# Kernel tuning notes

Measured on AMD Instinct MI355X. Metric: run time of the kernel, lower is better.

## Reference

```python
import jax, jax.numpy as jnp
import numpy as np
from jax import lax

B, T, C, H, W = 2, 5, 2, 128, 256
E, M, L = 64, 16, 4  # embedding_dim, n_fno_modes, n_fno_layers
EPS = 1e-5


def conv1x1(x, w, b):
    # x: [N, I, H, W], w: [O, I], b: [O]
    return jnp.einsum('nihw,oi->nohw', x, w) + b[None, :, None, None]


def conv3x3(x, w, b):
    # x: [N, I, H, W], w: [O, I, 3, 3]
    y = lax.conv_general_dilated(x, w, window_strides=(1, 1), padding='SAME',
                                 dimension_numbers=('NCHW', 'OIHW', 'NCHW'))
    return y + b[None, :, None, None]


def instance_norm(x):
    # InstanceNorm2d(affine=False): normalize over H,W per (n, c), biased var
    mu = jnp.mean(x, axis=(2, 3), keepdims=True)
    var = jnp.var(x, axis=(2, 3), keepdims=True)
    return (x - mu) * lax.rsqrt(var + EPS)


def upsample2x_nearest(x):
    return jnp.repeat(jnp.repeat(x, 2, axis=2), 2, axis=3)


def resize_nearest(x, out_h, out_w):
    # torch F.interpolate mode='nearest': idx = floor(i * in / out)
    in_h, in_w = x.shape[2], x.shape[3]
    hi = (jnp.arange(out_h) * in_h) // out_h
    wi = (jnp.arange(out_w) * in_w) // out_w
    return x[:, :, hi, :][:, :, :, wi]


def fno_layer(x, wr, wi, cw, cb):
    # x: [N, E, H, W]; wr/wi: [2, E, E, M, M]; cw: [E, E]; cb: [E]
    h, w = x.shape[2], x.shape[3]
    coeff = jnp.fft.rfft2(x, axes=(2, 3), norm='ortho')  # [N, E, H, W//2+1]
    w0 = wr[0] + 1j * wi[0]
    w1 = wr[1] + 1j * wi[1]
    out = jnp.zeros_like(coeff)
    out = out.at[:, :, :M, :M].set(
        jnp.einsum('nixy,ioxy->noxy', coeff[:, :, :M, :M], w0))
    out = out.at[:, :, -M:, :M].set(
        jnp.einsum('nixy,ioxy->noxy', coeff[:, :, -M:, :M], w1))
    spec = jnp.fft.irfft2(out, s=(h, w), axes=(2, 3), norm='ortho')
    return jax.nn.gelu(conv1x1(x, cw, cb) + spec, approximate=False)


def setup_inputs() -> dict:
    key = jax.random.key(0)
    ks = jax.random.split(key, 10)
    s = 0.02
    return {
        'sensor_value': jax.random.normal(ks[0], (B, T, C, H, W), jnp.float32),
        'updim_w': 0.3 * jax.random.normal(ks[1], (E, C), jnp.float32),
        'updim_b': jnp.zeros((E,), jnp.float32),
        'smooth_w': 0.04 * jax.random.normal(ks[2], (E, E, 3, 3), jnp.float32),
        'smooth_b': jnp.zeros((E,), jnp.float32),
        'fno_wr': s * jax.random.normal(ks[3], (L, 2, E, E, M, M), jnp.float32),
        'fno_wi': s * jax.random.normal(ks[4], (L, 2, E, E, M, M), jnp.float32),
        'fno_cw': 0.1 * jax.random.normal(ks[5], (L, E, E), jnp.float32),
        'fno_cb': jnp.zeros((L, E), jnp.float32),
        'downdim_w': 0.1 * jax.random.normal(ks[6], (C, E), jnp.float32),
        'downdim_b': jnp.zeros((C,), jnp.float32),
    }


def reference(sensor_value, updim_w, updim_b, smooth_w, smooth_b,
              fno_wr, fno_wi, fno_cw, fno_cb, downdim_w, downdim_b):
    b, t, c, h, w = sensor_value.shape
    x = sensor_value.reshape(b * t, c, h, w)
    x = conv1x1(x, updim_w, updim_b)
    x = upsample2x_nearest(x)
    x = jax.nn.gelu(instance_norm(conv3x3(x, smooth_w, smooth_b)), approximate=False)
    x = resize_nearest(x, H, W)
    for l in range(L):
        x = fno_layer(x, fno_wr[l], fno_wi[l], fno_cw[l], fno_cb[l])
    x = conv1x1(x, downdim_w, downdim_b)
    return x.reshape(b, t, c, H, W)
```

## Files before the change

### kernel.cpp

```cpp
#include <hip/hip_runtime.h>
#include <math.h>

#define PI_D 3.14159265358979323846


typedef _Float16 h8 __attribute__((ext_vector_type(8)));
typedef float f16v __attribute__((ext_vector_type(16)));

__device__ __forceinline__ float gelu_f(float v){
  return 0.5f*v*(1.0f + erff(v*0.70710678118654752440f));
}

__device__ __forceinline__ int fsw_c(int w){ return (w ^ (w >> 3)) & 7; }

__global__ __launch_bounds__(256) void k_tables(float* __restrict__ twFwH, float* __restrict__ twBwH,
                                                _Float16* __restrict__ Tspec, _Float16* __restrict__ TdftW){
  int id = blockIdx.x*256 + threadIdx.x;
  if (id < 4096){
    int h = id >> 5, m = id & 31;
    int xm = (m < 16) ? m : (96 + m);
    double ang = -2.0*PI_D*(double)((xm*h) & 127)/128.0;
    twFwH[id*2]   = (float)cos(ang);
    twFwH[id*2+1] = (float)sin(ang);
  } else if (id < 8192){
    int j = id - 4096;
    int h = j >> 5, m = j & 31;
    int xm = (m < 16) ? m : (96 + m);
    double ang = 2.0*PI_D*(double)((xm*h) & 127)/128.0;
    twBwH[j*2]   = (float)cos(ang);
    twBwH[j*2+1] = (float)sin(ang);
  } else if (id < 16384){
    int j = id - 8192;
    int w = j >> 5, kk = j & 31;
    int y = kk >> 1;
    double ang = 2.0*PI_D*(double)((w*y) & 255)/256.0;
    double v = (kk & 1) ? -sin(ang) : cos(ang);
    Tspec[j] = (_Float16)v;
  } else if (id < 24576){
    int j = id - 16384;
    int y2 = j >> 8, w = j & 255;
    int y = y2 >> 1;
    double ang = -2.0*PI_D*(double)((w*y) & 255)/256.0;
    double v = (y2 & 1) ? sin(ang) : cos(ang);
    TdftW[j] = (_Float16)v;
  }
}

__global__ __launch_bounds__(256) void k_foldK(const float* __restrict__ smw, const float* __restrict__ upw,
                                               const float* __restrict__ upb, float* __restrict__ Keff){
  int id = blockIdx.x*256 + threadIdx.x;
  if (id >= 1024) return;
  int o = id >> 4, rs = (id >> 2) & 3, tap = id & 3;
  int r = rs >> 1, s = rs & 1, a = tap >> 1, b = tap & 1;
  int klo = (r==0) ? (a==0?0:1) : (a==0?0:2);
  int khi = (r==0) ? (a==0?0:2) : (a==0?1:2);
  int llo = (s==0) ? (b==0?0:1) : (b==0?0:2);
  int lhi = (s==0) ? (b==0?0:2) : (b==0?1:2);
  float a0=0.f, a1=0.f, ab=0.f;
  for (int i=0;i<64;++i){
    float t = 0.f;
    for (int kh=klo; kh<=khi; ++kh)
      for (int kw=llo; kw<=lhi; ++kw)
        t += smw[((size_t)o*64+i)*9 + kh*3+kw];
    a0 += t*upw[i*2];
    a1 += t*upw[i*2+1];
    ab += t*upb[i];
  }
  *(float4*)(Keff + o*64 + (rs*4+tap)*4) = make_float4(a0, a1, ab, 0.f);
}

__global__ __launch_bounds__(256) void k_transW(const float* __restrict__ wr, const float* __restrict__ wi,
                                                unsigned* __restrict__ Wt){
  __shared__ unsigned P[64*257];
  int lb = blockIdx.x;
  int i = lb & 63, blk = (lb>>6)&1, l = lb>>7;
  int tid = threadIdx.x;
  size_t sbase = (size_t)l*2097152 + (size_t)blk*1048576 + (size_t)i*16384 + tid;
  for (int o=0;o<64;++o){
    float a = wr[sbase + (size_t)o*256];
    float b = wi[sbase + (size_t)o*256];
    union { unsigned u; _Float16 h[2]; } pk;
    pk.h[0] = (_Float16)a; pk.h[1] = (_Float16)b;
    P[o*257 + tid] = pk.u;
  }
  __syncthreads();
  int o = tid & 63, g = tid >> 6;
  size_t dbase = (size_t)(l*2+blk)*1048576;
  for (int it=0; it<64; ++it){
    int my = g*64 + it;
    Wt[dbase + (size_t)my*4096 + i*64 + o] = P[o*257 + my];
  }
}

__global__ __launch_bounds__(512) void k_corr(const float* __restrict__ sv, float* __restrict__ Rpart){
  __shared__ float S[2][6][260];
  int bid = blockIdx.x;
  int band = bid & 31, n = bid >> 5;
  int u0 = band*4;
  int tid = threadIdx.x;
  for (int t = tid; t < 3120; t += 512){
    int ch = t / 1560; int rem = t - ch*1560; int rr = rem / 260; int ci = rem - rr*260;
    int row = u0 - 1 + rr, col = ci - 1;
    float v = 0.f;
    if (row >= 0 && row < 128 && col >= 0 && col < 256)
      v = sv[((size_t)(n*2+ch)*128 + row)*256 + col];
    S[ch][rr][ci] = v;
  }
  __syncthreads();

  int lane = tid & 63, wv = tid >> 6;
  int c  = (wv<4) ? (wv>>1) : ((wv<6) ? (wv-4) : 2);
  int c2 = (wv<4) ? (wv&1)  : ((wv<6) ? 2 : (wv-6));
  float acc[9];
  #pragma unroll
  for (int k=0;k<9;++k) acc[k]=0.f;

  for (int r=0;r<4;++r){
    int u = u0 + r, lu = r + 1;
    for (int cb=0;cb<4;++cb){
      int v = cb*64 + lane;
      float f = (c==2) ? 1.f : S[c][lu][1+v];
      #pragma unroll
      for (int dr=-1;dr<=1;++dr){
        int ur = u + dr;
        float rko = (ur>=0 && ur<128) ? 1.f : 0.f;
        #pragma unroll
        for (int dc=-1;dc<=1;++dc){
          float g;
          if (c2==2){
            int vc = v + dc;
            g = rko * ((vc>=0 && vc<256) ? 1.f : 0.f);
          } else {
            g = S[c2][lu+dr][1+v+dc];
          }
          acc[(dr+1)*3 + dc+1] += f*g;
        }
      }
    }
  }
  #pragma unroll
  for (int k=0;k<9;++k){
    float v = acc[k];
    for (int off=32; off; off>>=1) v += __shfl_xor(v, off);
    if (lane==0) Rpart[((size_t)(n*32+band)*8 + wv)*9 + k] = v;
  }
}

__global__ __launch_bounds__(256) void k_bnd(const float* __restrict__ sv, float* __restrict__ Bnd){
  __shared__ float E[4][3][260];
  int n = blockIdx.x, tid = threadIdx.x;
  for (int t = tid; t < 3120; t += 256){
    int e = t/780; int rem = t - e*780; int ch = rem/260; int i = rem - ch*260;
    int idx = i - 1;
    int len = (e<2) ? 256 : 128;
    float v = 0.f;
    if (idx >= 0 && idx < len){
      if (ch==2) v = 1.f;
      else {
        int row = (e==0) ? 0 : (e==1) ? 127 : idx;
        int col = (e==2) ? 0 : (e==3) ? 255 : idx;
        v = sv[((size_t)(n*2+ch)*128 + row)*256 + col];
      }
    }
    E[e][ch][i] = v;
  }
  __syncthreads();
  if (tid < 108){
    int e = tid/27; int rem = tid - e*27; int pair = rem/3; int lag = rem%3 - 1;
    int c = pair/3, c2 = pair%3;
    int len = (e<2) ? 256 : 128;
    float a = 0.f;
    for (int i=0;i<len;++i) a += E[e][c][1+i]*E[e][c2][1+i+lag];
    Bnd[n*144 + tid] = a;
  } else if (tid < 144){
    int t = tid - 108; int corner = t/9; int pair = t - corner*9;
    int c = pair/3, c2 = pair%3;
    int e = (corner<2) ? 0 : 1;
    int idx = (corner&1) ? 255 : 0;
    Bnd[n*144 + tid] = E[e][c][1+idx]*E[e][c2][1+idx];
  }
}

__global__ __launch_bounds__(256) void k_stats3(const float* __restrict__ Rpart, const float* __restrict__ Bnd,
                                                const float* __restrict__ Keff, float* __restrict__ stats){
  __shared__ float R[9][9];
  __shared__ float BL[4][9][3];
  __shared__ float CR[4][9];
  __shared__ float M[4][12][12];
  int n = blockIdx.x, tid = threadIdx.x;

  if (tid < 72){
    int wv = tid/9, k = tid - (tid/9)*9;
    double s = 0.0;
    for (int b=0;b<32;++b) s += (double)Rpart[((size_t)(n*32+b)*8 + wv)*9 + k];
    int c  = (wv<4) ? (wv>>1) : ((wv<6) ? (wv-4) : 2);
    int c2 = (wv<4) ? (wv&1)  : ((wv<6) ? 2 : (wv-6));
    R[c*3+c2][k] = (float)s;
  } else if (tid < 81){
    int k = tid - 72; int dr = k/3 - 1, dc = k%3 - 1;
    R[8][k] = (float)((128 - (dr<0?-dr:dr)) * (256 - (dc<0?-dc:dc)));
  }
  if (tid < 108){
    int e = tid/27, rem = tid - (tid/27)*27;
    BL[e][rem/3][rem%3] = Bnd[n*144 + tid];
  } else if (tid < 144){
    int t = tid - 108;
    CR[t/9][t - (t/9)*9] = Bnd[n*144 + tid];
  }
  __syncthreads();

  for (int t = tid; t < 576; t += 256){
    int rs = t/144; int rem = t - rs*144; int i = rem/12, j = rem - (rem/12)*12;
    int ab = i/3,  c  = i - ab*3,  a  = ab>>1, b  = ab&1;
    int ab2 = j/3, c2 = j - ab2*3, a2 = ab2>>1, b2 = ab2&1;
    int r = rs>>1, s = rs&1;
    int dr = a2 - a, dc = b2 - b;
    int pair = c*3 + c2;
    float g = R[pair][(dr+1)*3 + (dc+1)];
    if (r==1 && a==1 && a2==1) g -= BL[0][pair][dc+1];
    if (r==0 && a==0 && a2==0) g -= BL[1][pair][dc+1];
    if (s==1 && b==1 && b2==1) g -= BL[2][pair][dr+1];
    if (s==0 && b==0 && b2==0) g -= BL[3][pair][dr+1];
    bool rowc = (a==a2) && ((r==1 && a==1) || (r==0 && a==0));
    bool colc = (b==b2) && ((s==1 && b==1) || (s==0 && b==0));
    if (rowc && colc){
      int corner = ((r==1)?0:2) + ((s==1)?0:1);
      g += CR[corner][pair];
    }
    M[rs][i][j] = g;
  }
  __syncthreads();

  if (tid < 64){
    int o = tid;
    double S1 = 0.0, S2 = 0.0;
    for (int rs=0; rs<4; ++rs){
      float w[12];
      #pragma unroll
      for (int ab=0; ab<4; ++ab){
        float4 kv = *(const float4*)(Keff + o*64 + (rs*4+ab)*4);
        w[ab*3+0] = kv.x; w[ab*3+1] = kv.y; w[ab*3+2] = kv.z;
      }
      #pragma unroll
      for (int i=0;i<12;++i){
        double ti = 0.0;
        #pragma unroll
        for (int j=0;j<12;++j) ti += (double)M[rs][i][j]*(double)w[j];
        S2 += (double)w[i]*ti;
      }
      #pragma unroll
      for (int ab=0; ab<4; ++ab)
        #pragma unroll
        for (int c=0;c<3;++c)
          S1 += (double)w[ab*3+c]*(double)M[rs][ab*3+c][ab*3+2];
    }
    double mu  = S1 / 131072.0;
    double var = S2 / 131072.0 - mu*mu;
    stats[(n*64+o)*2]   = (float)mu;
    stats[(n*64+o)*2+1] = (float)(1.0/sqrt(var + 1e-5));
  }
}

__global__ __launch_bounds__(256) void k_convnorm(const float* __restrict__ sv,
                                                  const float* __restrict__ Keff,
                                                  const float* __restrict__ stats,
                                                  _Float16* __restrict__ act){
  __shared__ float SV[4*260];
  int bid = blockIdx.x;
  int p = bid & 127, n = bid >> 7;
  int tid = threadIdx.x;
  for (int t = tid; t < 1032; t += 256){
    int dr = t / 516;
    int rem = t - dr*516;
    int ch = rem / 258;
    int ci = rem - ch*258;
    int row = p - 1 + dr;
    int col = ci - 1;
    float v = 0.f;
    if (row >= 0 && col >= 0 && col < 256)
      v = sv[((size_t)(n*2+ch)*128 + row)*256 + col];
    SV[(dr*2+ch)*260 + ci] = v;
  }
  __syncthreads();

  int q = tid;
  float x0[4], x1[4], ib[4];
  float rowok0 = (p>0)?1.f:0.f;
  float colok0 = (q>0)?1.f:0.f;
  #pragma unroll
  for (int a=0;a<2;++a)
    #pragma unroll
    for (int b=0;b<2;++b){
      x0[a*2+b] = SV[(a*2+0)*260 + q + b];
      x1[a*2+b] = SV[(a*2+1)*260 + q + b];
      ib[a*2+b] = (a==0?rowok0:1.f) * (b==0?colok0:1.f);
    }

  for (int o=0; o<64; ++o){
    const float4* kp = (const float4*)(Keff + o*64);
    float y = 0.f;
    #pragma unroll
    for (int t=0;t<4;++t){
      float4 kv = kp[t];
      y += kv.x*x0[t] + kv.y*x1[t] + kv.z*ib[t];
    }
    float mu = stats[(n*64+o)*2], istd = stats[(n*64+o)*2+1];
    float v = (y - mu)*istd;
    act[((size_t)(n*64+o)*128 + p)*256 + q] = (_Float16)gelu_f(v);
  }
}

__global__ __launch_bounds__(256, 2) void k_dftW_mfma(const _Float16* __restrict__ act,
                                                      const _Float16* __restrict__ TdftW,
                                                      float* __restrict__ Cy){
  __shared__ _Float16 Ax[32768];
  __shared__ _Float16 Bt[8192];
  int tid = threadIdx.x;
  int hp = blockIdx.x & 63, n = blockIdx.x >> 6;
  int h0 = hp*2;

  {
    int a = tid >> 1;
    int ws = (tid & 1) * 128;
    int e = a & 63, ht = a >> 6;
    const _Float16* src = act + ((size_t)(n*64+e))*32768 + (size_t)(h0+ht)*256 + ws;
    #pragma unroll
    for (int k=0;k<16;++k){
      h8 v = *(const h8*)(src + k*8);
      int wq = (ws >> 3) + k;
      int chunk = wq ^ (a & 7);
      *(h8*)(Ax + a*256 + chunk*8) = v;
    }
  }
  {
    int y2 = tid & 31, ws = (tid >> 5) * 32;
    const _Float16* src = TdftW + y2*256 + ws;
    #pragma unroll
    for (int k=0;k<4;++k){
      h8 v = *(const h8*)(src + k*8);
      int wq = (ws >> 3) + k;
      int chunk = wq ^ (y2 & 7);
      *(h8*)(Bt + y2*256 + chunk*8) = v;
    }
  }
  __syncthreads();

  int lane = tid & 63;
  int l31 = lane & 31, l5 = lane >> 5;
  int mt = tid >> 6;
  int a = mt*32 + l31;

  f16v acc;
  #pragma unroll
  for (int j=0;j<16;++j) acc[j] = 0.f;
  #pragma unroll
  for (int ks=0;ks<16;++ks){
    int kb = ks*16 + l5*8;
    int cA = (kb>>3) ^ (a & 7);
    int cB = (kb>>3) ^ (l31 & 7);
    h8 af = *(const h8*)(Ax + a*256 + cA*8);
    h8 bf = *(const h8*)(Bt + l31*256 + cB*8);
    acc = __builtin_amdgcn_mfma_f32_32x32x16_f16(bf, af, acc, 0,0,0);
  }
  int e = a & 63, ht = a >> 6;
  #pragma unroll
  for (int j=0;j<16;j+=2){
    int y2 = (j&3) + 8*(j>>2) + 4*l5;
    int yy = y2 >> 1;
    *(float2*)(Cy + (((size_t)(n*16+yy)*128 + h0+ht)*64 + e)*2) = make_float2(acc[j], acc[j+1]);
  }
}

__global__ __launch_bounds__(256) void k_specAB(const float* __restrict__ Cy,
                                                const float* __restrict__ twF,
                                                const unsigned* __restrict__ Wt,
                                                float* __restrict__ MS, int l){
  __shared__ float CO[8*64*2];
  int bid = blockIdx.x;
  int mq = bid / 160;
  int pid = bid - mq*160;
  int y = pid & 15, n = pid >> 4;
  int tid = threadIdx.x;
  int lane = tid & 63;
  int wv = __builtin_amdgcn_readfirstlane(tid >> 6);

  {
    int m0 = mq*8 + wv*2;
    const float* cyb = Cy + (((size_t)(n*16+y)*128)*64 + lane)*2;
    const float* tf = twF + m0*2;
    float ar0=0.f, ai0=0.f, ar1=0.f, ai1=0.f;
    for (int h=0; h<128; ++h){
      float2 c = *(const float2*)(cyb + h*128);
      const float* tp = tf + h*64;
      float t0r = tp[0], t0i = tp[1], t1r = tp[2], t1i = tp[3];
      ar0 += t0r*c.x - t0i*c.y; ai0 += t0r*c.y + t0i*c.x;
      ar1 += t1r*c.x - t1i*c.y; ai1 += t1r*c.y + t1i*c.x;
    }
    int mm = wv*2;
    *(float2*)(CO + (mm*64 + lane)*2)     = make_float2(ar0, ai0);
    *(float2*)(CO + ((mm+1)*64 + lane)*2) = make_float2(ar1, ai1);
  }
  __syncthreads();

  {
    #pragma unroll
    for (int t2=0; t2<2; ++t2){
      int mm = wv*2 + t2;
      int m = mq*8 + mm;
      int blk = m >> 4, mloc = m & 15;
      int my = mloc*16 + y;
      const unsigned* wb = Wt + ((size_t)((l*2+blk)*256 + my))*4096 + lane;
      float mr = 0.f, mi = 0.f;
      for (int i=0;i<64;++i){
        float2 cc = *(const float2*)(CO + (mm*64 + i)*2);
        union { unsigned u; _Float16 h[2]; } pk;
        pk.u = wb[(size_t)i*64];
        float wr_f = (float)pk.h[0], wi_f = (float)pk.h[1];
        mr += cc.x*wr_f - cc.y*wi_f;
        mi += cc.x*wi_f + cc.y*wr_f;
      }
      *(float2*)(MS + (((size_t)(n*16+y)*32 + m)*64 + lane)*2) = make_float2(mr, mi);
    }
  }
}

__global__ __launch_bounds__(256) void k_specC(const float* __restrict__ MS,
                                               const float* __restrict__ twB,
                                               float* __restrict__ G){
  __shared__ float SM[32*64*2];
  int bid = blockIdx.x;
  int hq = bid / 160;
  int pid = bid - hq*160;
  int y = pid & 15, n = pid >> 4;
  int tid = threadIdx.x;
  int lane = tid & 63;
  int wv = __builtin_amdgcn_readfirstlane(tid >> 6);

  {
    const float4* src = (const float4*)(MS + ((size_t)(n*16+y)*32)*128);
    float4* dst = (float4*)SM;
    #pragma unroll
    for (int t=0; t<4; ++t) dst[tid + t*256] = src[tid + t*256];
  }
  __syncthreads();

  float f = (y==0) ? (1.f/32768.f) : (2.f/32768.f);
  for (int k=0;k<8;++k){
    int h = hq*32 + wv*8 + k;
    const float* tb = twB + h*64;
    float gr=0.f, gi=0.f;
    #pragma unroll
    for (int m=0;m<32;++m){
      float tr = tb[m*2], ti = tb[m*2+1];
      float2 mo2 = *(const float2*)(SM + (m*64+lane)*2);
      gr += tr*mo2.x - ti*mo2.y;
      gi += tr*mo2.y + ti*mo2.x;
    }
    size_t gb = (((size_t)(n*128+h)*16 + y)*2)*64 + lane;
    G[gb]      = gr*f;
    G[gb + 64] = gi*f;
  }
}

__global__ __launch_bounds__(512, 4) void k_combine_mfma(const _Float16* __restrict__ act_in,
                                                         const float* __restrict__ G,
                                                         const _Float16* __restrict__ Tspec,
                                                         const float* __restrict__ cw,
                                                         const float* __restrict__ cb,
                                                         _Float16* __restrict__ act_out){
  __shared__ _Float16 Bx[32768];
  __shared__ _Float16 At[8192];
  int tid = threadIdx.x;
  int h = blockIdx.x & 127, n = blockIdx.x >> 7;

  {
    int rp = tid >> 4, sub = tid & 15;
    int i0 = 2*rp;
    int wbase = sub*16;
    const _Float16* r0 = act_in + (size_t)(n*64+i0)*32768 + (size_t)h*256 + wbase;
    const _Float16* r1 = r0 + 32768;
    h8 A0 = *(const h8*)r0,     A1 = *(const h8*)(r0+8);
    h8 B0 = *(const h8*)r1,     B1 = *(const h8*)(r1+8);
    int cbs = rp >> 2;
    int lo  = i0 & 7;
    #pragma unroll
    for (int k=0;k<16;++k){
      union { _Float16 hh[2]; unsigned u; } pk;
      pk.hh[0] = (k<8) ? A0[k] : A1[k-8];
      pk.hh[1] = (k<8) ? B0[k] : B1[k-8];
      int w = wbase + k;
      int chunk = cbs ^ fsw_c(w);
      *(unsigned*)(Bx + w*128 + chunk*8 + lo) = pk.u;
    }
  }
  {
    int o = tid >> 3, seg = (tid & 7)*8;
    float4 c0 = *(const float4*)(cw + o*64 + seg);
    float4 c1 = *(const float4*)(cw + o*64 + seg + 4);
    h8 v;
    v[0]=(_Float16)c0.x; v[1]=(_Float16)c0.y; v[2]=(_Float16)c0.z; v[3]=(_Float16)c0.w;
    v[4]=(_Float16)c1.x; v[5]=(_Float16)c1.y; v[6]=(_Float16)c1.z; v[7]=(_Float16)c1.w;
    int ch0 = (seg>>3) ^ (o & 7);
    *(h8*)(At + o*128 + ch0*8) = v;
  }
  {
    const float* gp = G + (size_t)(n*128 + h)*2048 + tid*4;
    float4 g = *(const float4*)gp;
    float gv[4] = {g.x, g.y, g.z, g.w};
    int idx0 = tid*4;
    int yc = idx0 >> 6;
    int o0 = idx0 & 63;
    int kk = 64 + yc;
    #pragma unroll
    for (int j=0;j<4;++j){
      int o = o0 + j;
      int chunk = (kk >> 3) ^ (o & 7);
      At[o*128 + chunk*8 + (kk & 7)] = (_Float16)gv[j];
    }
  }
  {
    int w = tid >> 1, half = tid & 1;
    const _Float16* tp = Tspec + w*32 + half*16;
    #pragma unroll
    for (int c=0;c<2;++c){
      h8 v = *(const h8*)(tp + c*8);
      int cc = half*2 + c;
      int chunk = (8 + cc) ^ fsw_c(w);
      *(h8*)(Bx + w*128 + chunk*8) = v;
    }
  }
  __syncthreads();

  int lane = tid & 63;
  int l31 = lane & 31, l5 = lane >> 5;
  int w0i = tid >> 6;
  int mt = w0i & 1, ng = w0i >> 1;
  int o_lane = mt*32 + l31;

  h8 af[6];
  #pragma unroll
  for (int ks=0;ks<6;++ks){
    int kb = ks*16 + l5*8;
    int chunk = (kb>>3) ^ (o_lane & 7);
    af[ks] = *(const h8*)(At + o_lane*128 + chunk*8);
  }
  float bias[16];
  #pragma unroll
  for (int j=0;j<16;++j) bias[j] = cb[mt*32 + (j&3) + 8*(j>>2) + 4*l5];

  f16v acc[2];
  #pragma unroll
  for (int q=0;q<2;++q)
    #pragma unroll
    for (int j=0;j<16;++j) acc[q][j] = bias[j];

  #pragma unroll
  for (int q=0;q<2;++q){
    int w = (ng*2+q)*32 + l31;
    const _Float16* bbase = Bx + w*128;
    int wf = fsw_c(w);
    #pragma unroll
    for (int ks=0;ks<6;++ks){
      int kb = ks*16 + l5*8;
      int chunk = (kb>>3) ^ wf;
      h8 bf = *(const h8*)(bbase + chunk*8);
      acc[q] = __builtin_amdgcn_mfma_f32_32x32x16_f16(af[ks], bf, acc[q], 0,0,0);
    }
  }

  #pragma unroll
  for (int q=0;q<2;++q){
    int wcol = (ng*2+q)*32 + l31;
    #pragma unroll
    for (int j=0;j<16;++j){
      int o = mt*32 + (j&3) + 8*(j>>2) + 4*l5;
      float v = gelu_f(acc[q][j]);
      act_out[(size_t)(n*64+o)*32768 + (size_t)h*256 + wcol] = (_Float16)v;
    }
  }
}

__global__ __launch_bounds__(256) void k_downdim(const _Float16* __restrict__ x, const float* __restrict__ wd,
                                                 const float* __restrict__ bd, float* __restrict__ out){
  size_t idx = (size_t)blockIdx.x*256 + threadIdx.x;
  int n = (int)(idx >> 15);
  int pos = (int)(idx & 32767);
  float a0 = bd[0], a1 = bd[1];
  const _Float16* xp = x + (size_t)n*2097152 + pos;
  for (int e=0;e<64;++e){
    float v = (float)xp[(size_t)e*32768];
    a0 += wd[e]*v;
    a1 += wd[64+e]*v;
  }
  out[(size_t)n*65536 + pos] = a0;
  out[(size_t)n*65536 + 32768 + pos] = a1;
}

extern "C" void kernel_launch(void* const* d_in, const int* in_sizes, int n_in,
                              void* d_out, int out_size, void* d_ws, size_t ws_size,
                              hipStream_t stream) {
  const float* sv  = (const float*)d_in[0];
  const float* upw = (const float*)d_in[1];
  const float* upb = (const float*)d_in[2];
  const float* smw = (const float*)d_in[3];
  const float* smb = (const float*)d_in[4];
  const float* fwr = (const float*)d_in[5];
  const float* fwi = (const float*)d_in[6];
  const float* fcw = (const float*)d_in[7];
  const float* fcb = (const float*)d_in[8];
  const float* ddw = (const float*)d_in[9];
  const float* ddb = (const float*)d_in[10];
  float* out = (float*)d_out;
  (void)smb;

  float* W = (float*)d_ws;
  _Float16* actA = (_Float16*)W;
  _Float16* actB = (_Float16*)(W + 10485760);
  float* Cy    = W + 20971520;
  float* G     = W + 23592960;
  float* part  = W + 26214400;
  float* stats = W + 28180480;
  float* Keff  = W + 28181760;
  float* twFwH = W + 28185856;
  float* twBwH = W + 28194048;
  _Float16* Tspec = (_Float16*)(W + 28202240);
  _Float16* TdftW = (_Float16*)(W + 28206336);
  unsigned* Wt   = (unsigned*)(W + 28210432);

  float* Rpart = part;
  float* Bnd   = part + 30000;
  float* MS    = part + 65536;

  k_tables<<<96,256,0,stream>>>(twFwH, twBwH, Tspec, TdftW);
  k_foldK<<<4,256,0,stream>>>(smw, upw, upb, Keff);
  k_transW<<<512,256,0,stream>>>(fwr, fwi, Wt);
  k_corr<<<320,512,0,stream>>>(sv, Rpart);
  k_bnd<<<10,256,0,stream>>>(sv, Bnd);
  k_stats3<<<10,256,0,stream>>>(Rpart, Bnd, Keff, stats);
  k_convnorm<<<1280,256,0,stream>>>(sv, Keff, stats, actA);

  _Float16* xa = actA; _Float16* xb = actB;
  for (int l=0;l<4;++l){
    k_dftW_mfma<<<640,256,0,stream>>>(xa, TdftW, Cy);
    k_specAB<<<640,256,0,stream>>>(Cy, twFwH, Wt, MS, l);
    k_specC<<<640,256,0,stream>>>(MS, twBwH, G);
    k_combine_mfma<<<1280,512,0,stream>>>(xa, G, Tspec, fcw + (size_t)l*4096, fcb + (size_t)l*64, xb);
    _Float16* t = xa; xa = xb; xb = t;
  }
  k_downdim<<<1280,256,0,stream>>>(xa, ddw, ddb, out);
}
```

Baseline: 493.9 us.

## Fuse next-layer W-direction DFT and final downdim into combine kernel

Each block of the combine kernel now takes its freshly computed GELU output rows, stages them in LDS and runs the next layer's W-direction DFT with MFMA, writing Cy directly. On the last layer it computes the 2-channel downdim projection in-register and writes the final output without storing the activation. Several small setup kernels (tables/foldK, corr/bnd) are merged into single launches. This removes the separate dftW kernel launches, the downdim kernel, and the re-reading of activations from global memory. In exchange the combine kernel gains extra LDS traffic, additional barriers and register pressure.

Measured after the change: 460.7 us. -6.7%, faster.

```diff
diff --git a/kernel.cpp b/kernel.cpp
--- a/kernel.cpp
+++ b/kernel.cpp
@@ -13,60 +13,62 @@
 
 __device__ __forceinline__ int fsw_c(int w){ return (w ^ (w >> 3)) & 7; }
 
-__global__ __launch_bounds__(256) void k_tables(float* __restrict__ twFwH, float* __restrict__ twBwH,
-                                                _Float16* __restrict__ Tspec, _Float16* __restrict__ TdftW){
-  int id = blockIdx.x*256 + threadIdx.x;
-  if (id < 4096){
-    int h = id >> 5, m = id & 31;
-    int xm = (m < 16) ? m : (96 + m);
-    double ang = -2.0*PI_D*(double)((xm*h) & 127)/128.0;
-    twFwH[id*2]   = (float)cos(ang);
-    twFwH[id*2+1] = (float)sin(ang);
-  } else if (id < 8192){
-    int j = id - 4096;
-    int h = j >> 5, m = j & 31;
-    int xm = (m < 16) ? m : (96 + m);
-    double ang = 2.0*PI_D*(double)((xm*h) & 127)/128.0;
-    twBwH[j*2]   = (float)cos(ang);
-    twBwH[j*2+1] = (float)sin(ang);
-  } else if (id < 16384){
-    int j = id - 8192;
-    int w = j >> 5, kk = j & 31;
-    int y = kk >> 1;
-    double ang = 2.0*PI_D*(double)((w*y) & 255)/256.0;
-    double v = (kk & 1) ? -sin(ang) : cos(ang);
-    Tspec[j] = (_Float16)v;
-  } else if (id < 24576){
-    int j = id - 16384;
-    int y2 = j >> 8, w = j & 255;
-    int y = y2 >> 1;
-    double ang = -2.0*PI_D*(double)((w*y) & 255)/256.0;
-    double v = (y2 & 1) ? sin(ang) : cos(ang);
-    TdftW[j] = (_Float16)v;
-  }
-}
-
-__global__ __launch_bounds__(256) void k_foldK(const float* __restrict__ smw, const float* __restrict__ upw,
-                                               const float* __restrict__ upb, float* __restrict__ Keff){
-  int id = blockIdx.x*256 + threadIdx.x;
-  if (id >= 1024) return;
-  int o = id >> 4, rs = (id >> 2) & 3, tap = id & 3;
-  int r = rs >> 1, s = rs & 1, a = tap >> 1, b = tap & 1;
-  int klo = (r==0) ? (a==0?0:1) : (a==0?0:2);
-  int khi = (r==0) ? (a==0?0:2) : (a==0?1:2);
-  int llo = (s==0) ? (b==0?0:1) : (b==0?0:2);
-  int lhi = (s==0) ? (b==0?0:2) : (b==0?1:2);
-  float a0=0.f, a1=0.f, ab=0.f;
-  for (int i=0;i<64;++i){
-    float t = 0.f;
-    for (int kh=klo; kh<=khi; ++kh)
-      for (int kw=llo; kw<=lhi; ++kw)
-        t += smw[((size_t)o*64+i)*9 + kh*3+kw];
-    a0 += t*upw[i*2];
-    a1 += t*upw[i*2+1];
-    ab += t*upb[i];
-  }
-  *(float4*)(Keff + o*64 + (rs*4+tap)*4) = make_float4(a0, a1, ab, 0.f);
+__global__ __launch_bounds__(256) void k_tables_fold(float* __restrict__ twFwH, float* __restrict__ twBwH,
+                                                     _Float16* __restrict__ Tspec, _Float16* __restrict__ TdftW,
+                                                     const float* __restrict__ smw, const float* __restrict__ upw,
+                                                     const float* __restrict__ upb, float* __restrict__ Keff){
+  int bid = blockIdx.x;
+  if (bid < 96){
+    int id = bid*256 + threadIdx.x;
+    if (id < 4096){
+      int h = id >> 5, m = id & 31;
+      int xm = (m < 16) ? m : (96 + m);
+      double ang = -2.0*PI_D*(double)((xm*h) & 127)/128.0;
+      twFwH[id*2]   = (float)cos(ang);
+      twFwH[id*2+1] = (float)sin(ang);
+    } else if (id < 8192){
+      int j = id - 4096;
+      int h = j >> 5, m = j & 31;
+      int xm = (m < 16) ? m : (96 + m);
+      double ang = 2.0*PI_D*(double)((xm*h) & 127)/128.0;
+      twBwH[j*2]   = (float)cos(ang);
+      twBwH[j*2+1] = (float)sin(ang);
+    } else if (id < 16384){
+      int j = id - 8192;
+      int w = j >> 5, kk = j & 31;
+      int y = kk >> 1;
+      double ang = 2.0*PI_D*(double)((w*y) & 255)/256.0;
+      double v = (kk & 1) ? -sin(ang) : cos(ang);
+      Tspec[j] = (_Float16)v;
+    } else if (id < 24576){
+      int j = id - 16384;
+      int y2 = j >> 8, w = j & 255;
+      int y = y2 >> 1;
+      double ang = -2.0*PI_D*(double)((w*y) & 255)/256.0;
+      double v = (y2 & 1) ? sin(ang) : cos(ang);
+      TdftW[j] = (_Float16)v;
+    }
+  } else {
+    int id = (bid-96)*256 + threadIdx.x;
+    if (id >= 1024) return;
+    int o = id >> 4, rs = (id >> 2) & 3, tap = id & 3;
+    int r = rs >> 1, s = rs & 1, a = tap >> 1, b = tap & 1;
+    int klo = (r==0) ? (a==0?0:1) : (a==0?0:2);
+    int khi = (r==0) ? (a==0?0:2) : (a==0?1:2);
+    int llo = (s==0) ? (b==0?0:1) : (b==0?0:2);
+    int lhi = (s==0) ? (b==0?0:2) : (b==0?1:2);
+    float a0=0.f, a1=0.f, ab=0.f;
+    for (int i=0;i<64;++i){
+      float t = 0.f;
+      for (int kh=klo; kh<=khi; ++kh)
+        for (int kw=llo; kw<=lhi; ++kw)
+          t += smw[((size_t)o*64+i)*9 + kh*3+kw];
+      a0 += t*upw[i*2];
+      a1 += t*upw[i*2+1];
+      ab += t*upb[i];
+    }
+    *(float4*)(Keff + o*64 + (rs*4+tap)*4) = make_float4(a0, a1, ab, 0.f);
+  }
 }
 
 __global__ __launch_bounds__(256) void k_transW(const float* __restrict__ wr, const float* __restrict__ wi,
@@ -92,92 +94,92 @@
   }
 }
 
-__global__ __launch_bounds__(512) void k_corr(const float* __restrict__ sv, float* __restrict__ Rpart){
-  __shared__ float S[2][6][260];
+__global__ __launch_bounds__(512) void k_corrbnd(const float* __restrict__ sv, float* __restrict__ Rpart,
+                                                 float* __restrict__ Bnd){
+  __shared__ float SH[3120];
   int bid = blockIdx.x;
-  int band = bid & 31, n = bid >> 5;
-  int u0 = band*4;
   int tid = threadIdx.x;
-  for (int t = tid; t < 3120; t += 512){
-    int ch = t / 1560; int rem = t - ch*1560; int rr = rem / 260; int ci = rem - rr*260;
-    int row = u0 - 1 + rr, col = ci - 1;
-    float v = 0.f;
-    if (row >= 0 && row < 128 && col >= 0 && col < 256)
-      v = sv[((size_t)(n*2+ch)*128 + row)*256 + col];
-    S[ch][rr][ci] = v;
-  }
-  __syncthreads();
-
-  int lane = tid & 63, wv = tid >> 6;
-  int c  = (wv<4) ? (wv>>1) : ((wv<6) ? (wv-4) : 2);
-  int c2 = (wv<4) ? (wv&1)  : ((wv<6) ? 2 : (wv-6));
-  float acc[9];
-  #pragma unroll
-  for (int k=0;k<9;++k) acc[k]=0.f;
-
-  for (int r=0;r<4;++r){
-    int u = u0 + r, lu = r + 1;
-    for (int cb=0;cb<4;++cb){
-      int v = cb*64 + lane;
-      float f = (c==2) ? 1.f : S[c][lu][1+v];
-      #pragma unroll
-      for (int dr=-1;dr<=1;++dr){
-        int ur = u + dr;
-        float rko = (ur>=0 && ur<128) ? 1.f : 0.f;
+  if (bid < 320){
+    int band = bid & 31, n = bid >> 5;
+    int u0 = band*4;
+    for (int t = tid; t < 3120; t += 512){
+      int ch = t / 1560; int rem = t - ch*1560; int rr = rem / 260; int ci = rem - rr*260;
+      int row = u0 - 1 + rr, col = ci - 1;
+      float v = 0.f;
+      if (row >= 0 && row < 128 && col >= 0 && col < 256)
+        v = sv[((size_t)(n*2+ch)*128 + row)*256 + col];
+      SH[(ch*6+rr)*260 + ci] = v;
+    }
+    __syncthreads();
+
+    int lane = tid & 63, wv = tid >> 6;
+    int c  = (wv<4) ? (wv>>1) : ((wv<6) ? (wv-4) : 2);
+    int c2 = (wv<4) ? (wv&1)  : ((wv<6) ? 2 : (wv-6));
+    float acc[9];
+    #pragma unroll
+    for (int k=0;k<9;++k) acc[k]=0.f;
+
+    for (int r=0;r<4;++r){
+      int u = u0 + r, lu = r + 1;
+      for (int cb=0;cb<4;++cb){
+        int v = cb*64 + lane;
+        float f = (c==2) ? 1.f : SH[(c*6+lu)*260 + 1+v];
         #pragma unroll
-        for (int dc=-1;dc<=1;++dc){
-          float g;
-          if (c2==2){
-            int vc = v + dc;
-            g = rko * ((vc>=0 && vc<256) ? 1.f : 0.f);
-          } else {
-            g = S[c2][lu+dr][1+v+dc];
+        for (int dr=-1;dr<=1;++dr){
+          int ur = u + dr;
+          float rko = (ur>=0 && ur<128) ? 1.f : 0.f;
+          #pragma unroll
+          for (int dc=-1;dc<=1;++dc){
+            float g;
+            if (c2==2){
+              int vc = v + dc;
+              g = rko * ((vc>=0 && vc<256) ? 1.f : 0.f);
+            } else {
+              g = SH[(c2*6+lu+dr)*260 + 1+v+dc];
+            }
+            acc[(dr+1)*3 + dc+1] += f*g;
           }
-          acc[(dr+1)*3 + dc+1] += f*g;
         }
       }
     }
-  }
-  #pragma unroll
-  for (int k=0;k<9;++k){
-    float v = acc[k];
-    for (int off=32; off; off>>=1) v += __shfl_xor(v, off);
-    if (lane==0) Rpart[((size_t)(n*32+band)*8 + wv)*9 + k] = v;
-  }
-}
-
-__global__ __launch_bounds__(256) void k_bnd(const float* __restrict__ sv, float* __restrict__ Bnd){
-  __shared__ float E[4][3][260];
-  int n = blockIdx.x, tid = threadIdx.x;
-  for (int t = tid; t < 3120; t += 256){
-    int e = t/780; int rem = t - e*780; int ch = rem/260; int i = rem - ch*260;
-    int idx = i - 1;
-    int len = (e<2) ? 256 : 128;
-    float v = 0.f;
-    if (idx >= 0 && idx < len){
-      if (ch==2) v = 1.f;
-      else {
-        int row = (e==0) ? 0 : (e==1) ? 127 : idx;
-        int col = (e==2) ? 0 : (e==3) ? 255 : idx;
-        v = sv[((size_t)(n*2+ch)*128 + row)*256 + col];
-      }
-    }
-    E[e][ch][i] = v;
-  }
-  __syncthreads();
-  if (tid < 108){
-    int e = tid/27; int rem = tid - e*27; int pair = rem/3; int lag = rem%3 - 1;
-    int c = pair/3, c2 = pair%3;
-    int len = (e<2) ? 256 : 128;
-    float a = 0.f;
-    for (int i=0;i<len;++i) a += E[e][c][1+i]*E[e][c2][1+i+lag];
-    Bnd[n*144 + tid] = a;
-  } else if (tid < 144){
-    int t = tid - 108; int corner = t/9; int pair = t - corner*9;
-    int c = pair/3, c2 = pair%3;
-    int e = (corner<2) ? 0 : 1;
-    int idx = (corner&1) ? 255 : 0;
-    Bnd[n*144 + tid] = E[e][c][1+idx]*E[e][c2][1+idx];
+    #pragma unroll
+    for (int k=0;k<9;++k){
+      float v = acc[k];
+      for (int off=32; off; off>>=1) v += __shfl_xor(v, off);
+      if (lane==0) Rpart[((size_t)(n*32+band)*8 + wv)*9 + k] = v;
+    }
+  } else {
+    int n = bid - 320;
+    for (int t = tid; t < 3120; t += 512){
+      int e = t/780; int rem = t - e*780; int ch = rem/260; int i = rem - ch*260;
+      int idx = i - 1;
+      int len = (e<2) ? 256 : 128;
+      float v = 0.f;
+      if (idx >= 0 && idx < len){
+        if (ch==2) v = 1.f;
+        else {
+          int row = (e==0) ? 0 : (e==1) ? 127 : idx;
+          int col = (e==2) ? 0 : (e==3) ? 255 : idx;
+          v = sv[((size_t)(n*2+ch)*128 + row)*256 + col];
+        }
+      }
+      SH[(e*3+ch)*260 + i] = v;
+    }
+    __syncthreads();
+    if (tid < 108){
+      int e = tid/27; int rem = tid - e*27; int pair = rem/3; int lag = rem%3 - 1;
+      int c = pair/3, c2 = pair%3;
+      int len = (e<2) ? 256 : 128;
+      float a = 0.f;
+      for (int i=0;i<len;++i) a += SH[(e*3+c)*260 + 1+i]*SH[(e*3+c2)*260 + 1+i+lag];
+      Bnd[n*144 + tid] = a;
+    } else if (tid < 144){
+      int t = tid - 108; int corner = t/9; int pair = t - corner*9;
+      int c = pair/3, c2 = pair%3;
+      int e = (corner<2) ? 0 : 1;
+      int idx = (corner&1) ? 255 : 0;
+      Bnd[n*144 + tid] = SH[(e*3+c)*260 + 1+idx]*SH[(e*3+c2)*260 + 1+idx];
+    }
   }
 }
 
@@ -465,11 +467,18 @@
 __global__ __launch_bounds__(512, 4) void k_combine_mfma(const _Float16* __restrict__ act_in,
                                                          const float* __restrict__ G,
                                                          const _Float16* __restrict__ Tspec,
+                                                         const _Float16* __restrict__ TdftW,
                                                          const float* __restrict__ cw,
                                                          const float* __restrict__ cb,
-                                                         _Float16* __restrict__ act_out){
-  __shared__ _Float16 Bx[32768];
-  __shared__ _Float16 At[8192];
+                                                         const float* __restrict__ wd,
+                                                         const float* __restrict__ bd,
+                                                         _Float16* __restrict__ act_out,
+                                                         float* __restrict__ Cy,
+                                                         float* __restrict__ outp,
+                                                         int flags){
+  __shared__ __align__(16) _Float16 Lh[40960];
+  _Float16* Bx = Lh;
+  _Float16* At = Lh + 32768;
   int tid = threadIdx.x;
   int h = blockIdx.x & 127, n = blockIdx.x >> 7;
 
@@ -506,7 +515,7 @@
   {
     const float* gp = G + (size_t)(n*128 + h)*2048 + tid*4;
     float4 g = *(const float4*)gp;
-    float gv[4] = {g.x, g.y, g.z, g.w};
+    float gvx[4] = {g.x, g.y, g.z, g.w};
     int idx0 = tid*4;
     int yc = idx0 >> 6;
     int o0 = idx0 & 63;
@@ -515,7 +524,7 @@
     for (int j=0;j<4;++j){
       int o = o0 + j;
       int chunk = (kk >> 3) ^ (o & 7);
-      At[o*128 + chunk*8 + (kk & 7)] = (_Float16)gv[j];
+      At[o*128 + chunk*8 + (kk & 7)] = (_Float16)gvx[j];
     }
   }
   {
@@ -568,32 +577,102 @@
     }
   }
 
-  #pragma unroll
-  for (int q=0;q<2;++q){
-    int wcol = (ng*2+q)*32 + l31;
+  float gvv[32];
+  #pragma unroll
+  for (int q=0;q<2;++q)
+    #pragma unroll
+    for (int j=0;j<16;++j) gvv[q*16+j] = gelu_f(acc[q][j]);
+
+  if (flags != 2){
+    #pragma unroll
+    for (int q=0;q<2;++q){
+      int wcol = (ng*2+q)*32 + l31;
+      #pragma unroll
+      for (int j=0;j<16;++j){
+        int o = mt*32 + (j&3) + 8*(j>>2) + 4*l5;
+        act_out[(size_t)(n*64+o)*32768 + (size_t)h*256 + wcol] = (_Float16)gvv[q*16+j];
+      }
+    }
+  }
+  __syncthreads();
+
+  if (flags == 1){
+    _Float16* gL  = Lh;
+    _Float16* TdL = Lh + 16384;
+    #pragma unroll
+    for (int q=0;q<2;++q){
+      int wcol = (ng*2+q)*32 + l31;
+      int wc3 = wcol >> 3, wc7 = wcol & 7;
+      #pragma unroll
+      for (int j=0;j<16;++j){
+        int o = mt*32 + (j&3) + 8*(j>>2) + 4*l5;
+        gL[o*256 + ((wc3 ^ (o & 7))*8) + wc7] = (_Float16)gvv[q*16+j];
+      }
+    }
+    {
+      int y2 = tid & 31, ws = (tid >> 5)*16;
+      const _Float16* src = TdftW + y2*256 + ws;
+      #pragma unroll
+      for (int k=0;k<2;++k){
+        h8 v = *(const h8*)(src + k*8);
+        int chunk = ((ws>>3)+k) ^ (y2 & 7);
+        *(h8*)(TdL + y2*256 + chunk*8) = v;
+      }
+    }
+    __syncthreads();
+    float* P = (float*)(Lh + 32768);
+    if (w0i < 4){
+      int mt2 = w0i & 1, kh = w0i >> 1;
+      int ocol = mt2*32 + l31;
+      f16v acc2;
+      #pragma unroll
+      for (int j=0;j<16;++j) acc2[j] = 0.f;
+      #pragma unroll
+      for (int ks=0;ks<8;++ks){
+        int kb = (kh*8+ks)*16 + l5*8;
+        h8 af2 = *(const h8*)(gL  + ocol*256 + (((kb>>3) ^ (ocol & 7))*8));
+        h8 bf2 = *(const h8*)(TdL + l31*256  + (((kb>>3) ^ (l31 & 7))*8));
+        acc2 = __builtin_amdgcn_mfma_f32_32x32x16_f16(bf2, af2, acc2, 0,0,0);
+      }
+      #pragma unroll
+      for (int j=0;j<16;++j){
+        int y2 = (j&3) + 8*(j>>2) + 4*l5;
+        P[w0i*1024 + y2*32 + l31] = acc2[j];
+      }
+    }
+    __syncthreads();
+    #pragma unroll
+    for (int rep=0;rep<2;++rep){
+      int t = rep*512 + tid;
+      int yy = t >> 6, o = t & 63, mt2 = o >> 5, o31 = o & 31;
+      float re = P[mt2*1024 + (2*yy)*32 + o31]   + P[(2+mt2)*1024 + (2*yy)*32 + o31];
+      float im = P[mt2*1024 + (2*yy+1)*32 + o31] + P[(2+mt2)*1024 + (2*yy+1)*32 + o31];
+      *(float2*)(Cy + (((size_t)(n*16+yy)*128 + h)*64 + o)*2) = make_float2(re, im);
+    }
+  } else {
+    float p00=0.f,p01=0.f,p10=0.f,p11=0.f;
     #pragma unroll
     for (int j=0;j<16;++j){
       int o = mt*32 + (j&3) + 8*(j>>2) + 4*l5;
-      float v = gelu_f(acc[q][j]);
-      act_out[(size_t)(n*64+o)*32768 + (size_t)h*256 + wcol] = (_Float16)v;
-    }
-  }
-}
-
-__global__ __launch_bounds__(256) void k_downdim(const _Float16* __restrict__ x, const float* __restrict__ wd,
-                                                 const float* __restrict__ bd, float* __restrict__ out){
-  size_t idx = (size_t)blockIdx.x*256 + threadIdx.x;
-  int n = (int)(idx >> 15);
-  int pos = (int)(idx & 32767);
-  float a0 = bd[0], a1 = bd[1];
-  const _Float16* xp = x + (size_t)n*2097152 + pos;
-  for (int e=0;e<64;++e){
-    float v = (float)xp[(size_t)e*32768];
-    a0 += wd[e]*v;
-    a1 += wd[64+e]*v;
-  }
-  out[(size_t)n*65536 + pos] = a0;
-  out[(size_t)n*65536 + 32768 + pos] = a1;
+      float w0d = wd[o], w1d = wd[64+o];
+      p00 += w0d*gvv[j];     p10 += w1d*gvv[j];
+      p01 += w0d*gvv[16+j];  p11 += w1d*gvv[16+j];
+    }
+    p00 += __shfl_xor(p00,32); p10 += __shfl_xor(p10,32);
+    p01 += __shfl_xor(p01,32); p11 += __shfl_xor(p11,32);
+    float* red = (float*)(Lh + 32768);
+    if (l5 == 0){
+      int wa = (ng*2+0)*32 + l31, wb2 = (ng*2+1)*32 + l31;
+      red[wa*4  + mt*2 + 0] = p00; red[wa*4  + mt*2 + 1] = p10;
+      red[wb2*4 + mt*2 + 0] = p01; red[wb2*4 + mt*2 + 1] = p11;
+    }
+    __syncthreads();
+    {
+      int ch = tid >> 8, wcol = tid & 255;
+      float v = red[wcol*4 + ch] + red[wcol*4 + 2 + ch] + bd[ch];
+      outp[(size_t)n*65536 + (size_t)ch*32768 + (size_t)h*256 + wcol] = v;
+    }
+  }
 }
 
 extern "C" void kernel_launch(void* const* d_in, const int* in_sizes, int n_in,
@@ -631,21 +710,20 @@
   float* Bnd   = part + 30000;
   float* MS    = part + 65536;
 
-  k_tables<<<96,256,0,stream>>>(twFwH, twBwH, Tspec, TdftW);
-  k_foldK<<<4,256,0,stream>>>(smw, upw, upb, Keff);
+  k_tables_fold<<<100,256,0,stream>>>(twFwH, twBwH, Tspec, TdftW, smw, upw, upb, Keff);
   k_transW<<<512,256,0,stream>>>(fwr, fwi, Wt);
-  k_corr<<<320,512,0,stream>>>(sv, Rpart);
-  k_bnd<<<10,256,0,stream>>>(sv, Bnd);
+  k_corrbnd<<<330,512,0,stream>>>(sv, Rpart, Bnd);
   k_stats3<<<10,256,0,stream>>>(Rpart, Bnd, Keff, stats);
   k_convnorm<<<1280,256,0,stream>>>(sv, Keff, stats, actA);
+  k_dftW_mfma<<<640,256,0,stream>>>(actA, TdftW, Cy);
 
   _Float16* xa = actA; _Float16* xb = actB;
   for (int l=0;l<4;++l){
-    k_dftW_mfma<<<640,256,0,stream>>>(xa, TdftW, Cy);
     k_specAB<<<640,256,0,stream>>>(Cy, twFwH, Wt, MS, l);
     k_specC<<<640,256,0,stream>>>(MS, twBwH, G);
-    k_combine_mfma<<<1280,512,0,stream>>>(xa, G, Tspec, fcw + (size_t)l*4096, fcb + (size_t)l*64, xb);
+    k_combine_mfma<<<1280,512,0,stream>>>(xa, G, Tspec, TdftW,
+                                          fcw + (size_t)l*4096, fcb + (size_t)l*64,
+                                          ddw, ddb, xb, Cy, out, (l<3)?1:2);
     _Float16* t = xa; xa = xb; xb = t;
   }
-  k_downdim<<<1280,256,0,stream>>>(xa, ddw, ddb, out);
-}
+}
```
